# Performance work log

Hardware: AMD Instinct MI355X
Metric: run time of the kernel (lower is better)

The kernel has to match this reference:

```python
import jax, jax.numpy as jnp
import numpy as np

N_NODES = 100000
N_EDGES = 1600000
D_IN = 128
D_HID = 128
D_OUT = 40
N_LAYERS = 3
EPS = 1e-12


def setup_inputs() -> dict:
    key = jax.random.key(0)
    ks = jax.random.split(key, 12)
    s = 1.0 / np.sqrt(D_HID)
    return {
        "x": jax.random.normal(ks[0], (N_NODES, D_IN), jnp.float32),
        "edge_index": jax.random.randint(ks[1], (2, N_EDGES), 0, N_NODES, jnp.int64),
        "Wl": jax.random.uniform(ks[2], (N_LAYERS, D_HID, D_HID), jnp.float32, -s, s),
        "bl": jax.random.uniform(ks[3], (N_LAYERS, D_HID), jnp.float32, -s, s),
        "Wr": jax.random.uniform(ks[4], (N_LAYERS, D_HID, D_HID), jnp.float32, -s, s),
        "br": jax.random.uniform(ks[5], (N_LAYERS, D_HID), jnp.float32, -s, s),
        "W_post1": jax.random.uniform(ks[6], (D_HID, D_HID), jnp.float32, -s, s),
        "b_post1": jax.random.uniform(ks[7], (D_HID,), jnp.float32, -s, s),
        "W_post2": jax.random.uniform(ks[8], (D_OUT, D_HID), jnp.float32, -s, s),
        "b_post2": jax.random.uniform(ks[9], (D_OUT,), jnp.float32, -s, s),
    }


def reference(x, edge_index, Wl, bl, Wr, br, W_post1, b_post1, W_post2, b_post2):
    src, dst = edge_index[0], edge_index[1]
    n = x.shape[0]
    h = x
    for i in range(N_LAYERS):
        # scatter-add aggregation of neighbor features (MessagePassing aggr='add')
        prop = jax.ops.segment_sum(h[src], dst, num_segments=n)  # [N, D]
        out = h @ Wl[i].T + bl[i] + prop @ Wr[i].T + br[i]
        # F.normalize(out, p=2) along dim=1
        norm = jnp.linalg.norm(out, axis=1, keepdims=True)
        out = out / jnp.maximum(norm, EPS)
        h = jax.nn.relu(out)  # dropout p=0 -> identity
    h = h @ W_post1.T + b_post1
    h = h @ W_post2.T + b_post2
    return jax.nn.log_softmax(h, axis=1)
```

## Files before the change

### kernel.cpp

```cpp
#include <hip/hip_runtime.h>
#include <hip/hip_bf16.h>
#include <cstdint>
#include <cstddef>

#define NN 100000
#define DD 128
#define NE 1600000
#define NPB 196
#define NBUCK 511
#define BCAP 6144
#define BUCKCAP 4608
#define SCHUNK 8192

#if defined(__HIP_DEVICE_COMPILE__) && defined(__has_builtin)
# if __has_builtin(__builtin_amdgcn_cvt_pk_f32_fp8) && __has_builtin(__builtin_amdgcn_cvt_pk_fp8_f32)
#  define DEV_CVT8 1
# endif
#endif
#ifndef DEV_CVT8
# define DEV_CVT8 0
#endif

typedef short bf16x8 __attribute__((ext_vector_type(8)));
typedef float f32x4 __attribute__((ext_vector_type(4)));
typedef unsigned short u16;
typedef unsigned int u32;
typedef unsigned char u8;

__device__ inline float b2f(u16 u) {
    union { u32 i; float f; } c; c.i = ((u32)u) << 16; return c.f;
}
__device__ inline u16 f2b(float f) {
    __hip_bfloat16 h = __float2bfloat16(f);
    return *reinterpret_cast<u16*>(&h);
}

__device__ inline u32 enc1_fp8(float v) {
#if DEV_CVT8
    return 0;
#else
    float a = fabsf(v);
    if (a > 448.0f) a = 448.0f;
    u32 sgn = (v < 0.0f) ? 0x80u : 0u;
    if (a < 0.015625f) {
        int q = (int)rintf(a * 512.0f);
        return sgn | (u32)q;
    }
    int ex;
    float mant = frexpf(a, &ex);
    int m = (int)rintf(mant * 16.0f) - 8;
    int e = ex - 1 + 7;
    if (m == 8) { m = 0; e += 1; }
    if (e > 15) { e = 15; m = 6; }
    return sgn | ((u32)e << 3) | (u32)m;
#endif
}

__device__ inline u32 pack4_fp8(float a, float b, float c, float d) {
#if DEV_CVT8
    u32 r = 0;
    r = (u32)__builtin_amdgcn_cvt_pk_fp8_f32(a, b, (int)r, false);
    r = (u32)__builtin_amdgcn_cvt_pk_fp8_f32(c, d, (int)r, true);
    return r;
#else
    return enc1_fp8(a) | (enc1_fp8(b) << 8) | (enc1_fp8(c) << 16) | (enc1_fp8(d) << 24);
#endif
}

__device__ inline float dec1_fp8(u32 byte) {
    u32 lo = byte & 0x7Fu;
    union { u32 i; float f; } c;
    c.i = lo ? (((byte & 0x80u) << 24) | ((lo + 912u) << 20)) : 0u;
    return c.f;
}

__global__ __launch_bounds__(256)
void initcur_kernel(int* __restrict__ cur) {
    int t = blockIdx.x * 256 + threadIdx.x;
    if (t < NBUCK) cur[t] = t * BUCKCAP;
}

__global__ __launch_bounds__(256)
void bscatter_kernel(const int* __restrict__ ei, int* __restrict__ cursor,
                     u32* __restrict__ packed, int n_edges) {
    __shared__ int hist[NBUCK];
    const int tid = threadIdx.x;
    const int nchunks = (n_edges + SCHUNK - 1) / SCHUNK;
    for (int ch = blockIdx.x; ch < nchunks; ch += gridDim.x) {
        const int e0 = ch * SCHUNK;
        const int e1 = min(e0 + SCHUNK, n_edges);
        for (int i = tid; i < NBUCK; i += 256) hist[i] = 0;
        __syncthreads();
        for (int e = e0 + tid; e < e1; e += 256)
            atomicAdd(&hist[ei[n_edges + e] / NPB], 1);
        __syncthreads();
        for (int i = tid; i < NBUCK; i += 256) {
            int c = hist[i];
            hist[i] = (c > 0) ? atomicAdd(&cursor[i], c) : 0;
        }
        __syncthreads();
        for (int e = e0 + tid; e < e1; e += 256) {
            int s = ei[e];
            int d = ei[n_edges + e];
            int b = d / NPB;
            int ld = d - b * NPB;
            int pos = atomicAdd(&hist[b], 1);
            packed[pos] = ((u32)ld << 17) | (u32)s;
        }
        __syncthreads();
    }
}

__global__ __launch_bounds__(256)
void blocal_kernel(const u32* __restrict__ packed, const int* __restrict__ cursor,
                   int* __restrict__ row_ptr, int* __restrict__ rpe,
                   int* __restrict__ ssrc) {
    __shared__ int out_s[BCAP];
    __shared__ int cur_s[NPB];
    __shared__ int excl_s[NPB];
    __shared__ int ws[4];
    __shared__ int wexc[4];

    const int b = blockIdx.x;
    const int tid = threadIdx.x;
    const int lane = tid & 63, wv = tid >> 6;
    const int pbase = b * BUCKCAP;
    const int cnt = cursor[b] - pbase;

    if (tid < NPB) cur_s[tid] = 0;
    __syncthreads();
    for (int i = tid; i < cnt; i += 256)
        atomicAdd(&cur_s[packed[pbase + i] >> 17], 1);
    __syncthreads();

    int v = (tid < NPB) ? cur_s[tid] : 0;
    int inc = v;
    #pragma unroll
    for (int o = 1; o < 64; o <<= 1) {
        int u = __shfl_up(inc, o);
        if (lane >= o) inc += u;
    }
    if (lane == 63) ws[wv] = inc;
    __syncthreads();
    if (tid == 0) {
        int s = 0;
        #pragma unroll
        for (int k = 0; k < 4; ++k) { wexc[k] = s; s += ws[k]; }
    }
    __syncthreads();
    int excl = inc - v + wexc[wv];
    if (tid < NPB) excl_s[tid] = excl;
    int gnode = b * NPB + tid;
    if (tid < NPB && gnode < NN) {
        row_ptr[gnode] = pbase + excl;
        rpe[gnode] = pbase + excl + v;
    }
    __syncthreads();
    if (tid < NPB) cur_s[tid] = excl_s[tid];
    __syncthreads();

    if (cnt <= BCAP) {
        for (int i = tid; i < cnt; i += 256) {
            u32 p = packed[pbase + i];
            int pos = atomicAdd(&cur_s[p >> 17], 1);
            out_s[pos] = (int)(p & 0x1FFFF);
        }
        __syncthreads();
        for (int i = tid; i < cnt; i += 256) ssrc[pbase + i] = out_s[i];
    } else {
        for (int i = tid; i < cnt; i += 256) {
            u32 p = packed[pbase + i];
            int pos = atomicAdd(&cur_s[p >> 17], 1);
            ssrc[pbase + pos] = (int)(p & 0x1FFFF);
        }
    }
}

__global__ __launch_bounds__(256)
void cvt_x_kernel(const float* __restrict__ x, u16* __restrict__ xb,
                  u8* __restrict__ x8, long long n8) {
    long long t = (long long)blockIdx.x * blockDim.x + threadIdx.x;
    long long stride = (long long)gridDim.x * blockDim.x;
    for (; t < n8; t += stride) {
        float4 v0 = reinterpret_cast<const float4*>(x)[2 * t];
        float4 v1 = reinterpret_cast<const float4*>(x)[2 * t + 1];
        uint4 ob;
        ob.x = (u32)f2b(v0.x) | ((u32)f2b(v0.y) << 16);
        ob.y = (u32)f2b(v0.z) | ((u32)f2b(v0.w) << 16);
        ob.z = (u32)f2b(v1.x) | ((u32)f2b(v1.y) << 16);
        ob.w = (u32)f2b(v1.z) | ((u32)f2b(v1.w) << 16);
        reinterpret_cast<uint4*>(xb)[t] = ob;
        uint2 o8;
        o8.x = pack4_fp8(v0.x * 64.0f, v0.y * 64.0f, v0.z * 64.0f, v0.w * 64.0f);
        o8.y = pack4_fp8(v1.x * 64.0f, v1.y * 64.0f, v1.z * 64.0f, v1.w * 64.0f);
        reinterpret_cast<uint2*>(x8)[t] = o8;
    }
}

__global__ __launch_bounds__(256)
void cvt8_kernel(const u16* __restrict__ hb, u8* __restrict__ h8, int n8) {
    int t0 = blockIdx.x * 256 + threadIdx.x;
    int stride = gridDim.x * 256;
    for (int t = t0; t < n8; t += stride) {
        uint4 v = reinterpret_cast<const uint4*>(hb)[t];
        union { u32 i; float f; } c;
        float f0, f1, f2, f3, f4, f5, f6, f7;
        c.i = v.x << 16; f0 = c.f;  c.i = v.x & 0xffff0000u; f1 = c.f;
        c.i = v.y << 16; f2 = c.f;  c.i = v.y & 0xffff0000u; f3 = c.f;
        c.i = v.z << 16; f4 = c.f;  c.i = v.z & 0xffff0000u; f5 = c.f;
        c.i = v.w << 16; f6 = c.f;  c.i = v.w & 0xffff0000u; f7 = c.f;
        uint2 o;
        o.x = pack4_fp8(f0 * 64.0f, f1 * 64.0f, f2 * 64.0f, f3 * 64.0f);
        o.y = pack4_fp8(f4 * 64.0f, f5 * 64.0f, f6 * 64.0f, f7 * 64.0f);
        reinterpret_cast<uint2*>(h8)[t] = o;
    }
}

__global__ __launch_bounds__(256)
void cvt_w_kernel(const float* __restrict__ Wl, const float* __restrict__ Wr,
                  u16* __restrict__ Wcat) {
    int t = blockIdx.x * blockDim.x + threadIdx.x;
    const int NCAT = 3 * 128 * 256;
    if (t < NCAT) {
        int layer = t >> 15;
        int rem = t & 32767;
        int d = rem >> 8;
        int k = rem & 255;
        float v = (k < 128) ? Wl[layer * 16384 + d * 128 + k]
                            : Wr[layer * 16384 + d * 128 + (k - 128)];
        Wcat[t] = f2b(v);
    }
}

__global__ __launch_bounds__(256)
void wfuse_kernel(const float* __restrict__ W1f, const float* __restrict__ b1,
                  const float* __restrict__ W2, const float* __restrict__ b2,
                  u16* __restrict__ Wfb, float* __restrict__ bfuse) {
    int t = blockIdx.x * 256 + threadIdx.x;
    if (t < 48 * 128) {
        int l = t >> 7, k = t & 127;
        float s = 0.0f;
        if (l < 40) {
            for (int j = 0; j < 128; ++j)
                s += W2[l * 128 + j] * W1f[j * 128 + k];
        }
        Wfb[t] = f2b(s);
    }
    if (blockIdx.x == 0 && threadIdx.x < 40) {
        int l = threadIdx.x;
        float s = b2[l];
        for (int j = 0; j < 128; ++j) s += W2[l * 128 + j] * b1[j];
        bfuse[l] = s;
    }
}

#if DEV_CVT8
#define DEC8(q) do { \
    auto _p0 = __builtin_amdgcn_cvt_pk_f32_fp8((int)(q).x, false); \
    auto _p1 = __builtin_amdgcn_cvt_pk_f32_fp8((int)(q).x, true); \
    auto _p2 = __builtin_amdgcn_cvt_pk_f32_fp8((int)(q).y, false); \
    auto _p3 = __builtin_amdgcn_cvt_pk_f32_fp8((int)(q).y, true); \
    acc0 += _p0[0]; acc1 += _p0[1]; acc2 += _p1[0]; acc3 += _p1[1]; \
    acc4 += _p2[0]; acc5 += _p2[1]; acc6 += _p3[0]; acc7 += _p3[1]; \
} while (0)
#else
#define DEC8(q) do { \
    acc0 += dec1_fp8((q).x & 0xFFu); \
    acc1 += dec1_fp8(((q).x >> 8) & 0xFFu); \
    acc2 += dec1_fp8(((q).x >> 16) & 0xFFu); \
    acc3 += dec1_fp8((q).x >> 24); \
    acc4 += dec1_fp8((q).y & 0xFFu); \
    acc5 += dec1_fp8(((q).y >> 8) & 0xFFu); \
    acc6 += dec1_fp8(((q).y >> 16) & 0xFFu); \
    acc7 += dec1_fp8((q).y >> 24); \
} while (0)
#endif

__global__ __launch_bounds__(256)
void gather8_kernel(const u8* __restrict__ h8, const int* __restrict__ rp,
                    const int* __restrict__ rpe, const int* __restrict__ ssrc,
                    u16* __restrict__ prop, int n_nodes) {
    int wid = (blockIdx.x * blockDim.x + threadIdx.x) >> 6;
    int lane = threadIdx.x & 63;
    if (wid >= n_nodes) return;
    int beg = rp[wid], end = rpe[wid];
    int deg = end - beg;
    int nb = min(deg, 64);
    const int g = lane >> 4;
    const u8* hb = h8 + (lane & 15) * 8;

    float acc0 = 0, acc1 = 0, acc2 = 0, acc3 = 0;
    float acc4 = 0, acc5 = 0, acc6 = 0, acc7 = 0;

    int sv = (lane < nb) ? ssrc[beg + lane] : 0;

    int j = 0;
    for (; j + 15 < nb; j += 16) {
        int s0 = __shfl(sv, j + g);
        int s1 = __shfl(sv, j + 4 + g);
        int s2 = __shfl(sv, j + 8 + g);
        int s3 = __shfl(sv, j + 12 + g);
        uint2 v0 = *reinterpret_cast<const uint2*>(hb + (size_t)s0 * 128);
        uint2 v1 = *reinterpret_cast<const uint2*>(hb + (size_t)s1 * 128);
        uint2 v2 = *reinterpret_cast<const uint2*>(hb + (size_t)s2 * 128);
        uint2 v3 = *reinterpret_cast<const uint2*>(hb + (size_t)s3 * 128);
        DEC8(v0);
        DEC8(v1);
        DEC8(v2);
        DEC8(v3);
    }
    for (; j + 3 < nb; j += 4) {
        int s0 = __shfl(sv, j + g);
        uint2 v0 = *reinterpret_cast<const uint2*>(hb + (size_t)s0 * 128);
        DEC8(v0);
    }
    if (j < nb && g < nb - j) {
        int s0 = __shfl(sv, j + g);
        uint2 v0 = *reinterpret_cast<const uint2*>(hb + (size_t)s0 * 128);
        DEC8(v0);
    }
    for (int e = beg + 64 + g; e < end; e += 4) {
        int s0 = ssrc[e];
        uint2 v0 = *reinterpret_cast<const uint2*>(hb + (size_t)s0 * 128);
        DEC8(v0);
    }

    acc0 += __shfl_xor(acc0, 16); acc0 += __shfl_xor(acc0, 32);
    acc1 += __shfl_xor(acc1, 16); acc1 += __shfl_xor(acc1, 32);
    acc2 += __shfl_xor(acc2, 16); acc2 += __shfl_xor(acc2, 32);
    acc3 += __shfl_xor(acc3, 16); acc3 += __shfl_xor(acc3, 32);
    acc4 += __shfl_xor(acc4, 16); acc4 += __shfl_xor(acc4, 32);
    acc5 += __shfl_xor(acc5, 16); acc5 += __shfl_xor(acc5, 32);
    acc6 += __shfl_xor(acc6, 16); acc6 += __shfl_xor(acc6, 32);
    acc7 += __shfl_xor(acc7, 16); acc7 += __shfl_xor(acc7, 32);

    if (lane < 16) {
        const float us = 0.015625f;
        uint4 o;
        o.x = (u32)f2b(acc0 * us) | ((u32)f2b(acc1 * us) << 16);
        o.y = (u32)f2b(acc2 * us) | ((u32)f2b(acc3 * us) << 16);
        o.z = (u32)f2b(acc4 * us) | ((u32)f2b(acc5 * us) << 16);
        o.w = (u32)f2b(acc6 * us) | ((u32)f2b(acc7 * us) << 16);
        *reinterpret_cast<uint4*>(prop + (size_t)wid * DD + lane * 8) = o;
    }
}

__global__ __launch_bounds__(256)
void mfma_layer64(const u16* __restrict__ hin, const u16* __restrict__ prop,
                  const u16* __restrict__ Wc, const float* __restrict__ b1,
                  const float* __restrict__ b2, u16* __restrict__ out,
                  int n_nodes) {
    __shared__ char a_s[64 * 512];
    __shared__ float red_s[64][4];

    const int tid = threadIdx.x;
    const int w = tid >> 6;
    const int l = tid & 63;
    const int q = l >> 4;
    const int c16 = l & 15;

    bf16x8 bfrag[2][8];
    int col[2];
    float bias[2];
    #pragma unroll
    for (int t = 0; t < 2; ++t) {
        col[t] = w * 32 + t * 16 + c16;
        bias[t] = b1[col[t]] + b2[col[t]];
        #pragma unroll
        for (int kk = 0; kk < 8; ++kk)
            bfrag[t][kk] = *reinterpret_cast<const bf16x8*>(
                Wc + (size_t)col[t] * 256 + kk * 32 + q * 8);
    }

    const int base = blockIdx.x * 64;

    for (int ci = tid; ci < 2048; ci += 256) {
        int r = ci >> 5, c = ci & 31;
        int node = base + r;
        uint4 v = {0, 0, 0, 0};
        if (node < n_nodes) {
            const u16* src = (c < 16) ? (hin + (size_t)node * DD + c * 8)
                                      : (prop + (size_t)node * DD + (c - 16) * 8);
            v = *reinterpret_cast<const uint4*>(src);
        }
        *reinterpret_cast<uint4*>(a_s + r * 512 + ((c ^ (r & 7)) * 16)) = v;
    }
    __syncthreads();

    f32x4 acc[4][2] = {};
    #pragma unroll
    for (int kk = 0; kk < 8; ++kk) {
        int cc = kk * 4 + q;
        #pragma unroll
        for (int m = 0; m < 4; ++m) {
            int row = m * 16 + c16;
            bf16x8 a = *reinterpret_cast<const bf16x8*>(
                a_s + row * 512 + ((cc ^ (row & 7)) * 16));
            acc[m][0] = __builtin_amdgcn_mfma_f32_16x16x32_bf16(a, bfrag[0][kk], acc[m][0], 0, 0, 0);
            acc[m][1] = __builtin_amdgcn_mfma_f32_16x16x32_bf16(a, bfrag[1][kk], acc[m][1], 0, 0, 0);
        }
    }

    float vals[4][2][4];
    float ss[4][4];
    #pragma unroll
    for (int m = 0; m < 4; ++m) {
        #pragma unroll
        for (int reg = 0; reg < 4; ++reg) {
            float s = 0.0f;
            #pragma unroll
            for (int t = 0; t < 2; ++t) {
                float v = acc[m][t][reg] + bias[t];
                vals[m][t][reg] = v;
                s += v * v;
            }
            s += __shfl_xor(s, 1);
            s += __shfl_xor(s, 2);
            s += __shfl_xor(s, 4);
            s += __shfl_xor(s, 8);
            ss[m][reg] = s;
        }
    }
    if (c16 == 0) {
        #pragma unroll
        for (int m = 0; m < 4; ++m)
            #pragma unroll
            for (int reg = 0; reg < 4; ++reg)
                red_s[m * 16 + q * 4 + reg][w] = ss[m][reg];
    }
    __syncthreads();
    #pragma unroll
    for (int m = 0; m < 4; ++m) {
        #pragma unroll
        for (int reg = 0; reg < 4; ++reg) {
            int row = m * 16 + q * 4 + reg;
            float4 rr = *reinterpret_cast<float4*>(&red_s[row][0]);
            float tot = rr.x + rr.y + rr.z + rr.w;
            float rn = 1.0f / fmaxf(sqrtf(tot), 1e-12f);
            if (base + row < n_nodes) {
                #pragma unroll
                for (int t = 0; t < 2; ++t) {
                    float v = fmaxf(vals[m][t][reg] * rn, 0.0f);
                    out[(size_t)(base + row) * DD + col[t]] = f2b(v);
                }
            }
        }
    }
}

__global__ __launch_bounds__(256)
void postfused_kernel(const u16* __restrict__ hin, const u16* __restrict__ Wfb,
                      const float* __restrict__ bfuse, float* __restrict__ out,
                      int n_nodes) {
    __shared__ char a_s[64 * 256];
    const int tid = threadIdx.x;
    const int w = tid >> 6;
    const int l = tid & 63;
    const int q = l >> 4;
    const int c16 = l & 15;

    bf16x8 bfrag[3][4];
    float bias[3];
    int col[3];
    #pragma unroll
    for (int t = 0; t < 3; ++t) {
        col[t] = t * 16 + c16;
        bias[t] = (col[t] < 40) ? bfuse[col[t]] : 0.0f;
        #pragma unroll
        for (int kk = 0; kk < 4; ++kk)
            bfrag[t][kk] = *reinterpret_cast<const bf16x8*>(
                Wfb + col[t] * 128 + kk * 32 + q * 8);
    }

    const int base = blockIdx.x * 64;

    for (int ci = tid; ci < 1024; ci += 256) {
        int r = ci >> 4, c = ci & 15;
        uint4 v = {0, 0, 0, 0};
        if (base + r < n_nodes)
            v = *reinterpret_cast<const uint4*>(hin + (size_t)(base + r) * DD + c * 8);
        *reinterpret_cast<uint4*>(a_s + r * 256 + ((c ^ (r & 7)) * 16)) = v;
    }
    __syncthreads();

    f32x4 acc[3] = {};
    const int arow = w * 16 + c16;
    #pragma unroll
    for (int kk = 0; kk < 4; ++kk) {
        int cc = kk * 4 + q;
        bf16x8 a = *reinterpret_cast<const bf16x8*>(
            a_s + arow * 256 + ((cc ^ (arow & 7)) * 16));
        acc[0] = __builtin_amdgcn_mfma_f32_16x16x32_bf16(a, bfrag[0][kk], acc[0], 0, 0, 0);
        acc[1] = __builtin_amdgcn_mfma_f32_16x16x32_bf16(a, bfrag[1][kk], acc[1], 0, 0, 0);
        acc[2] = __builtin_amdgcn_mfma_f32_16x16x32_bf16(a, bfrag[2][kk], acc[2], 0, 0, 0);
    }

    #pragma unroll
    for (int reg = 0; reg < 4; ++reg) {
        int row = base + w * 16 + q * 4 + reg;
        float v[3];
        float m = -INFINITY;
        #pragma unroll
        for (int t = 0; t < 3; ++t) {
            v[t] = acc[t][reg] + bias[t];
            if (col[t] < 40) m = fmaxf(m, v[t]);
        }
        m = fmaxf(m, __shfl_xor(m, 1));
        m = fmaxf(m, __shfl_xor(m, 2));
        m = fmaxf(m, __shfl_xor(m, 4));
        m = fmaxf(m, __shfl_xor(m, 8));
        float s = 0.0f;
        #pragma unroll
        for (int t = 0; t < 3; ++t)
            if (col[t] < 40) s += expf(v[t] - m);
        s += __shfl_xor(s, 1);
        s += __shfl_xor(s, 2);
        s += __shfl_xor(s, 4);
        s += __shfl_xor(s, 8);
        float lg = logf(s);
        if (row < n_nodes) {
            #pragma unroll
            for (int t = 0; t < 3; ++t)
                if (col[t] < 40)
                    out[(size_t)row * 40 + col[t]] = v[t] - m - lg;
        }
    }
}

extern "C" void kernel_launch(void* const* d_in, const int* in_sizes, int n_in,
                              void* d_out, int out_size, void* d_ws, size_t ws_size,
                              hipStream_t stream) {
    const float* x   = (const float*)d_in[0];
    const int*   ei  = (const int*)d_in[1];
    const float* Wl  = (const float*)d_in[2];
    const float* bl  = (const float*)d_in[3];
    const float* Wr  = (const float*)d_in[4];
    const float* br  = (const float*)d_in[5];
    const float* W1f = (const float*)d_in[6];
    const float* b1  = (const float*)d_in[7];
    const float* W2  = (const float*)d_in[8];
    const float* b2  = (const float*)d_in[9];
    float* outp = (float*)d_out;

    u16* xb   = (u16*)d_ws;
    u16* P    = xb + (size_t)NN * DD;
    u16* bufA = P + (size_t)NN * DD;
    u16* bufB = bufA + (size_t)NN * DD;
    u8*  h8   = (u8*)(bufB + (size_t)NN * DD);
    u16* Wcat = (u16*)(h8 + (size_t)NN * 128);
    u16* Wfb  = Wcat + 3 * 128 * 256;
    float* bfuse = (float*)(Wfb + 8192);
    int* cursor  = (int*)(Wfb + 128 * 128);
    int* row_ptr = cursor + NBUCK + 1;
    int* rpe     = row_ptr + NN;
    int* ssrc    = rpe + NN;
    u32* packed  = (u32*)(ssrc + NBUCK * BUCKCAP);

    initcur_kernel<<<2, 256, 0, stream>>>(cursor);
    bscatter_kernel<<<(NE + SCHUNK - 1) / SCHUNK, 256, 0, stream>>>(
        ei, cursor, packed, NE);
    blocal_kernel<<<NBUCK, 256, 0, stream>>>(packed, cursor, row_ptr, rpe, ssrc);

    cvt_x_kernel<<<6250, 256, 0, stream>>>(x, xb, h8, (long long)NN * DD / 8);
    cvt_w_kernel<<<(3 * 128 * 256 + 255) / 256, 256, 0, stream>>>(Wl, Wr, Wcat);
    wfuse_kernel<<<24, 256, 0, stream>>>(W1f, b1, W2, b2, Wfb, bfuse);

    const int n_strips64 = (NN + 63) / 64;
    const int gather_grid = (NN * 64 + 255) / 256;
    const int n8 = NN * DD / 8;

    const u16* hcur = xb;
    u16* hnext;
    for (int i = 0; i < 3; ++i) {
        hnext = (i == 0) ? bufA : ((hcur == bufA) ? bufB : bufA);
        gather8_kernel<<<gather_grid, 256, 0, stream>>>(
            h8, row_ptr, rpe, ssrc, P, NN);
        mfma_layer64<<<n_strips64, 256, 0, stream>>>(
            hcur, P, Wcat + (size_t)i * 128 * 256,
            bl + (size_t)i * DD, br + (size_t)i * DD, hnext, NN);
        if (i < 2)
            cvt8_kernel<<<2048, 256, 0, stream>>>(hnext, h8, n8);
        hcur = hnext;
    }
    postfused_kernel<<<n_strips64, 256, 0, stream>>>(hcur, Wfb, bfuse, outp, NN);
}
```

Measured before the change: 312.7 us.

## Fuse fp8 emission into layer GEMM and load operands directly from global

The separate cvt8 pass is removed. Each layer GEMM now encodes its normalized ReLU output to scaled fp8 in shared memory and writes it out as the next layer's gather source. The GEMM also drops the LDS staging of the A tile and the preloaded weight fragments, and instead loads A rows and weight fragments straight from global memory inside the k loop. This saves a kernel launch and a full read and write of the bf16 activations, but the unstaged loads may be less coalesced and more latency bound.

```diff
diff --git a/kernel.cpp b/kernel.cpp
--- a/kernel.cpp
+++ b/kernel.cpp
@@ -35,10 +35,7 @@
     return *reinterpret_cast<u16*>(&h);
 }
 
-__device__ inline u32 enc1_fp8(float v) {
-#if DEV_CVT8
-    return 0;
-#else
+__device__ inline u32 enc1_fp8_sw(float v) {
     float a = fabsf(v);
     if (a > 448.0f) a = 448.0f;
     u32 sgn = (v < 0.0f) ? 0x80u : 0u;
@@ -53,7 +50,6 @@
     if (m == 8) { m = 0; e += 1; }
     if (e > 15) { e = 15; m = 6; }
     return sgn | ((u32)e << 3) | (u32)m;
-#endif
 }
 
 __device__ inline u32 pack4_fp8(float a, float b, float c, float d) {
@@ -63,7 +59,16 @@
     r = (u32)__builtin_amdgcn_cvt_pk_fp8_f32(c, d, (int)r, true);
     return r;
 #else
-    return enc1_fp8(a) | (enc1_fp8(b) << 8) | (enc1_fp8(c) << 16) | (enc1_fp8(d) << 24);
+    return enc1_fp8_sw(a) | (enc1_fp8_sw(b) << 8) | (enc1_fp8_sw(c) << 16)
+         | (enc1_fp8_sw(d) << 24);
+#endif
+}
+
+__device__ inline u8 enc1b_fp8(float v) {
+#if DEV_CVT8
+    return (u8)((u32)__builtin_amdgcn_cvt_pk_fp8_f32(v, v, 0, false) & 0xFFu);
+#else
+    return (u8)enc1_fp8_sw(v);
 #endif
 }
 
@@ -194,25 +199,6 @@
         o8.x = pack4_fp8(v0.x * 64.0f, v0.y * 64.0f, v0.z * 64.0f, v0.w * 64.0f);
         o8.y = pack4_fp8(v1.x * 64.0f, v1.y * 64.0f, v1.z * 64.0f, v1.w * 64.0f);
         reinterpret_cast<uint2*>(x8)[t] = o8;
-    }
-}
-
-__global__ __launch_bounds__(256)
-void cvt8_kernel(const u16* __restrict__ hb, u8* __restrict__ h8, int n8) {
-    int t0 = blockIdx.x * 256 + threadIdx.x;
-    int stride = gridDim.x * 256;
-    for (int t = t0; t < n8; t += stride) {
-        uint4 v = reinterpret_cast<const uint4*>(hb)[t];
-        union { u32 i; float f; } c;
-        float f0, f1, f2, f3, f4, f5, f6, f7;
-        c.i = v.x << 16; f0 = c.f;  c.i = v.x & 0xffff0000u; f1 = c.f;
-        c.i = v.y << 16; f2 = c.f;  c.i = v.y & 0xffff0000u; f3 = c.f;
-        c.i = v.z << 16; f4 = c.f;  c.i = v.z & 0xffff0000u; f5 = c.f;
-        c.i = v.w << 16; f6 = c.f;  c.i = v.w & 0xffff0000u; f7 = c.f;
-        uint2 o;
-        o.x = pack4_fp8(f0 * 64.0f, f1 * 64.0f, f2 * 64.0f, f3 * 64.0f);
-        o.y = pack4_fp8(f4 * 64.0f, f5 * 64.0f, f6 * 64.0f, f7 * 64.0f);
-        reinterpret_cast<uint2*>(h8)[t] = o;
     }
 }
 
@@ -345,13 +331,14 @@
     }
 }
 
-__global__ __launch_bounds__(256)
-void mfma_layer64(const u16* __restrict__ hin, const u16* __restrict__ prop,
-                  const u16* __restrict__ Wc, const float* __restrict__ b1,
-                  const float* __restrict__ b2, u16* __restrict__ out,
-                  int n_nodes) {
-    __shared__ char a_s[64 * 512];
+template<int EMIT8>
+__global__ __launch_bounds__(256)
+void mfma_layer_direct(const u16* __restrict__ hin, const u16* __restrict__ prop,
+                       const u16* __restrict__ Wc, const float* __restrict__ b1,
+                       const float* __restrict__ b2, u16* __restrict__ out,
+                       u8* __restrict__ h8out, int n_nodes) {
     __shared__ float red_s[64][4];
+    __shared__ u8 h8_s[EMIT8 ? 64 * 128 : 16];
 
     const int tid = threadIdx.x;
     const int w = tid >> 6;
@@ -359,45 +346,40 @@
     const int q = l >> 4;
     const int c16 = l & 15;
 
-    bf16x8 bfrag[2][8];
     int col[2];
     float bias[2];
     #pragma unroll
     for (int t = 0; t < 2; ++t) {
         col[t] = w * 32 + t * 16 + c16;
         bias[t] = b1[col[t]] + b2[col[t]];
-        #pragma unroll
-        for (int kk = 0; kk < 8; ++kk)
-            bfrag[t][kk] = *reinterpret_cast<const bf16x8*>(
-                Wc + (size_t)col[t] * 256 + kk * 32 + q * 8);
     }
 
     const int base = blockIdx.x * 64;
-
-    for (int ci = tid; ci < 2048; ci += 256) {
-        int r = ci >> 5, c = ci & 31;
-        int node = base + r;
-        uint4 v = {0, 0, 0, 0};
-        if (node < n_nodes) {
-            const u16* src = (c < 16) ? (hin + (size_t)node * DD + c * 8)
-                                      : (prop + (size_t)node * DD + (c - 16) * 8);
-            v = *reinterpret_cast<const uint4*>(src);
-        }
-        *reinterpret_cast<uint4*>(a_s + r * 512 + ((c ^ (r & 7)) * 16)) = v;
-    }
-    __syncthreads();
+    int node_m[4];
+    #pragma unroll
+    for (int m = 0; m < 4; ++m)
+        node_m[m] = min(base + m * 16 + c16, n_nodes - 1);
 
     f32x4 acc[4][2] = {};
     #pragma unroll
     for (int kk = 0; kk < 8; ++kk) {
-        int cc = kk * 4 + q;
+        const int cc = kk * 4 + q;
+        bf16x8 a[4];
         #pragma unroll
         for (int m = 0; m < 4; ++m) {
-            int row = m * 16 + c16;
-            bf16x8 a = *reinterpret_cast<const bf16x8*>(
-                a_s + row * 512 + ((cc ^ (row & 7)) * 16));
-            acc[m][0] = __builtin_amdgcn_mfma_f32_16x16x32_bf16(a, bfrag[0][kk], acc[m][0], 0, 0, 0);
-            acc[m][1] = __builtin_amdgcn_mfma_f32_16x16x32_bf16(a, bfrag[1][kk], acc[m][1], 0, 0, 0);
+            const u16* p = (kk < 4)
+                ? (hin + (size_t)node_m[m] * DD + cc * 8)
+                : (prop + (size_t)node_m[m] * DD + (cc - 16) * 8);
+            a[m] = *reinterpret_cast<const bf16x8*>(p);
+        }
+        bf16x8 bf0 = *reinterpret_cast<const bf16x8*>(
+            Wc + (size_t)col[0] * 256 + kk * 32 + q * 8);
+        bf16x8 bf1 = *reinterpret_cast<const bf16x8*>(
+            Wc + (size_t)col[1] * 256 + kk * 32 + q * 8);
+        #pragma unroll
+        for (int m = 0; m < 4; ++m) {
+            acc[m][0] = __builtin_amdgcn_mfma_f32_16x16x32_bf16(a[m], bf0, acc[m][0], 0, 0, 0);
+            acc[m][1] = __builtin_amdgcn_mfma_f32_16x16x32_bf16(a[m], bf1, acc[m][1], 0, 0, 0);
         }
     }
 
@@ -437,13 +419,25 @@
             float4 rr = *reinterpret_cast<float4*>(&red_s[row][0]);
             float tot = rr.x + rr.y + rr.z + rr.w;
             float rn = 1.0f / fmaxf(sqrtf(tot), 1e-12f);
-            if (base + row < n_nodes) {
-                #pragma unroll
-                for (int t = 0; t < 2; ++t) {
-                    float v = fmaxf(vals[m][t][reg] * rn, 0.0f);
+            bool alive = (base + row < n_nodes);
+            #pragma unroll
+            for (int t = 0; t < 2; ++t) {
+                float v = fmaxf(vals[m][t][reg] * rn, 0.0f);
+                if (alive)
                     out[(size_t)(base + row) * DD + col[t]] = f2b(v);
-                }
+                if (EMIT8)
+                    h8_s[row * 128 + col[t]] = enc1b_fp8(v * 64.0f);
             }
+        }
+    }
+    if (EMIT8) {
+        __syncthreads();
+        for (int i = tid; i < 512; i += 256) {
+            int row = i >> 3;
+            int node = base + row;
+            if (node < n_nodes)
+                reinterpret_cast<uint4*>(h8out + (size_t)node * 128)[i & 7] =
+                    reinterpret_cast<const uint4*>(h8_s)[i];
         }
     }
 }
@@ -567,7 +561,6 @@
 
     const int n_strips64 = (NN + 63) / 64;
     const int gather_grid = (NN * 64 + 255) / 256;
-    const int n8 = NN * DD / 8;
 
     const u16* hcur = xb;
     u16* hnext;
@@ -575,11 +568,15 @@
         hnext = (i == 0) ? bufA : ((hcur == bufA) ? bufB : bufA);
         gather8_kernel<<<gather_grid, 256, 0, stream>>>(
             h8, row_ptr, rpe, ssrc, P, NN);
-        mfma_layer64<<<n_strips64, 256, 0, stream>>>(
-            hcur, P, Wcat + (size_t)i * 128 * 256,
-            bl + (size_t)i * DD, br + (size_t)i * DD, hnext, NN);
-        if (i < 2)
-            cvt8_kernel<<<2048, 256, 0, stream>>>(hnext, h8, n8);
+        if (i < 2) {
+            mfma_layer_direct<1><<<n_strips64, 256, 0, stream>>>(
+                hcur, P, Wcat + (size_t)i * 128 * 256,
+                bl + (size_t)i * DD, br + (size_t)i * DD, hnext, h8, NN);
+        } else {
+            mfma_layer_direct<0><<<n_strips64, 256, 0, stream>>>(
+                hcur, P, Wcat + (size_t)i * 128 * 256,
+                bl + (size_t)i * DD, br + (size_t)i * DD, hnext, h8, NN);
+        }
         hcur = hnext;
     }
     postfused_kernel<<<n_strips64, 256, 0, stream>>>(hcur, Wfb, bfuse, outp, NN);
```

Result: slower. 350.5 us (+12.1%).

## Fuse neighbor gather into MFMA layer kernel, aggregating directly into LDS

Applied to the files above, without the earlier changes.

Merges the separate per-node fp8 gather kernel into the layer GEMM kernel: each block gathers and sums neighbor rows for its 64 nodes, with 16 lanes per node, and writes the bf16 aggregate straight into the swizzled shared-memory A tile. This removes the global round trip of the prop buffer and one kernel launch per layer. In exchange, each wave handles 4 nodes per pass, 16 at a time, with only 16 lanes each, so gather parallelism and latency hiding within a block fall and degree imbalance stalls the MFMA phase. Also renames the software fp8 encoder.

```diff
diff --git a/kernel.cpp b/kernel.cpp
--- a/kernel.cpp
+++ b/kernel.cpp
@@ -35,10 +35,7 @@
     return *reinterpret_cast<u16*>(&h);
 }
 
-__device__ inline u32 enc1_fp8(float v) {
-#if DEV_CVT8
-    return 0;
-#else
+__device__ inline u32 enc1_fp8_sw(float v) {
     float a = fabsf(v);
     if (a > 448.0f) a = 448.0f;
     u32 sgn = (v < 0.0f) ? 0x80u : 0u;
@@ -53,7 +50,6 @@
     if (m == 8) { m = 0; e += 1; }
     if (e > 15) { e = 15; m = 6; }
     return sgn | ((u32)e << 3) | (u32)m;
-#endif
 }
 
 __device__ inline u32 pack4_fp8(float a, float b, float c, float d) {
@@ -63,7 +59,8 @@
     r = (u32)__builtin_amdgcn_cvt_pk_fp8_f32(c, d, (int)r, true);
     return r;
 #else
-    return enc1_fp8(a) | (enc1_fp8(b) << 8) | (enc1_fp8(c) << 16) | (enc1_fp8(d) << 24);
+    return enc1_fp8_sw(a) | (enc1_fp8_sw(b) << 8) | (enc1_fp8_sw(c) << 16)
+         | (enc1_fp8_sw(d) << 24);
 #endif
 }
 
@@ -277,80 +274,12 @@
 #endif
 
 __global__ __launch_bounds__(256)
-void gather8_kernel(const u8* __restrict__ h8, const int* __restrict__ rp,
-                    const int* __restrict__ rpe, const int* __restrict__ ssrc,
-                    u16* __restrict__ prop, int n_nodes) {
-    int wid = (blockIdx.x * blockDim.x + threadIdx.x) >> 6;
-    int lane = threadIdx.x & 63;
-    if (wid >= n_nodes) return;
-    int beg = rp[wid], end = rpe[wid];
-    int deg = end - beg;
-    int nb = min(deg, 64);
-    const int g = lane >> 4;
-    const u8* hb = h8 + (lane & 15) * 8;
-
-    float acc0 = 0, acc1 = 0, acc2 = 0, acc3 = 0;
-    float acc4 = 0, acc5 = 0, acc6 = 0, acc7 = 0;
-
-    int sv = (lane < nb) ? ssrc[beg + lane] : 0;
-
-    int j = 0;
-    for (; j + 15 < nb; j += 16) {
-        int s0 = __shfl(sv, j + g);
-        int s1 = __shfl(sv, j + 4 + g);
-        int s2 = __shfl(sv, j + 8 + g);
-        int s3 = __shfl(sv, j + 12 + g);
-        uint2 v0 = *reinterpret_cast<const uint2*>(hb + (size_t)s0 * 128);
-        uint2 v1 = *reinterpret_cast<const uint2*>(hb + (size_t)s1 * 128);
-        uint2 v2 = *reinterpret_cast<const uint2*>(hb + (size_t)s2 * 128);
-        uint2 v3 = *reinterpret_cast<const uint2*>(hb + (size_t)s3 * 128);
-        DEC8(v0);
-        DEC8(v1);
-        DEC8(v2);
-        DEC8(v3);
-    }
-    for (; j + 3 < nb; j += 4) {
-        int s0 = __shfl(sv, j + g);
-        uint2 v0 = *reinterpret_cast<const uint2*>(hb + (size_t)s0 * 128);
-        DEC8(v0);
-    }
-    if (j < nb && g < nb - j) {
-        int s0 = __shfl(sv, j + g);
-        uint2 v0 = *reinterpret_cast<const uint2*>(hb + (size_t)s0 * 128);
-        DEC8(v0);
-    }
-    for (int e = beg + 64 + g; e < end; e += 4) {
-        int s0 = ssrc[e];
-        uint2 v0 = *reinterpret_cast<const uint2*>(hb + (size_t)s0 * 128);
-        DEC8(v0);
-    }
-
-    acc0 += __shfl_xor(acc0, 16); acc0 += __shfl_xor(acc0, 32);
-    acc1 += __shfl_xor(acc1, 16); acc1 += __shfl_xor(acc1, 32);
-    acc2 += __shfl_xor(acc2, 16); acc2 += __shfl_xor(acc2, 32);
-    acc3 += __shfl_xor(acc3, 16); acc3 += __shfl_xor(acc3, 32);
-    acc4 += __shfl_xor(acc4, 16); acc4 += __shfl_xor(acc4, 32);
-    acc5 += __shfl_xor(acc5, 16); acc5 += __shfl_xor(acc5, 32);
-    acc6 += __shfl_xor(acc6, 16); acc6 += __shfl_xor(acc6, 32);
-    acc7 += __shfl_xor(acc7, 16); acc7 += __shfl_xor(acc7, 32);
-
-    if (lane < 16) {
-        const float us = 0.015625f;
-        uint4 o;
-        o.x = (u32)f2b(acc0 * us) | ((u32)f2b(acc1 * us) << 16);
-        o.y = (u32)f2b(acc2 * us) | ((u32)f2b(acc3 * us) << 16);
-        o.z = (u32)f2b(acc4 * us) | ((u32)f2b(acc5 * us) << 16);
-        o.w = (u32)f2b(acc6 * us) | ((u32)f2b(acc7 * us) << 16);
-        *reinterpret_cast<uint4*>(prop + (size_t)wid * DD + lane * 8) = o;
-    }
-}
-
-__global__ __launch_bounds__(256)
-void mfma_layer64(const u16* __restrict__ hin, const u16* __restrict__ prop,
-                  const u16* __restrict__ Wc, const float* __restrict__ b1,
-                  const float* __restrict__ b2, u16* __restrict__ out,
-                  int n_nodes) {
-    __shared__ char a_s[64 * 512];
+void fused_layer(const u16* __restrict__ hin, const u8* __restrict__ h8,
+                 const int* __restrict__ rp, const int* __restrict__ rpe,
+                 const int* __restrict__ ssrc, const u16* __restrict__ Wc,
+                 const float* __restrict__ b1, const float* __restrict__ b2,
+                 u16* __restrict__ out, int n_nodes) {
+    __shared__ __attribute__((aligned(16))) char a_s[64 * 512];
     __shared__ float red_s[64][4];
 
     const int tid = threadIdx.x;
@@ -359,6 +288,63 @@
     const int q = l >> 4;
     const int c16 = l & 15;
 
+    const int base = blockIdx.x * 64;
+
+    for (int ci = tid; ci < 1024; ci += 256) {
+        int r = ci >> 4, c = ci & 15;
+        int node = base + r;
+        uint4 v = {0, 0, 0, 0};
+        if (node < n_nodes)
+            v = *reinterpret_cast<const uint4*>(hin + (size_t)node * DD + c * 8);
+        *reinterpret_cast<uint4*>(a_s + r * 512 + ((c ^ (r & 7)) * 16)) = v;
+    }
+
+    {
+        const int gb = l & 48;
+        const int cl = c16;
+        const float us = 0.015625f;
+        for (int pass = 0; pass < 4; ++pass) {
+            int r = w * 16 + pass * 4 + q;
+            int n = min(base + r, n_nodes - 1);
+            int beg = rp[n];
+            int deg = rpe[n] - beg;
+            float acc0 = 0, acc1 = 0, acc2 = 0, acc3 = 0;
+            float acc4 = 0, acc5 = 0, acc6 = 0, acc7 = 0;
+            for (int c0 = 0; c0 < deg; c0 += 16) {
+                int rem = deg - c0;
+                int sv = (cl < rem) ? ssrc[beg + c0 + cl] : 0;
+                #pragma unroll
+                for (int k = 0; k < 16; k += 4) {
+                    if (k >= rem) break;
+                    int s0 = __shfl(sv, gb | k);
+                    int s1 = __shfl(sv, gb | (k + 1));
+                    int s2 = __shfl(sv, gb | (k + 2));
+                    int s3 = __shfl(sv, gb | (k + 3));
+                    uint2 v0, v1 = {0, 0}, v2 = {0, 0}, v3 = {0, 0};
+                    v0 = *reinterpret_cast<const uint2*>(h8 + (size_t)s0 * 128 + cl * 8);
+                    if (k + 1 < rem)
+                        v1 = *reinterpret_cast<const uint2*>(h8 + (size_t)s1 * 128 + cl * 8);
+                    if (k + 2 < rem)
+                        v2 = *reinterpret_cast<const uint2*>(h8 + (size_t)s2 * 128 + cl * 8);
+                    if (k + 3 < rem)
+                        v3 = *reinterpret_cast<const uint2*>(h8 + (size_t)s3 * 128 + cl * 8);
+                    DEC8(v0);
+                    DEC8(v1);
+                    DEC8(v2);
+                    DEC8(v3);
+                }
+            }
+            uint4 o;
+            o.x = (u32)f2b(acc0 * us) | ((u32)f2b(acc1 * us) << 16);
+            o.y = (u32)f2b(acc2 * us) | ((u32)f2b(acc3 * us) << 16);
+            o.z = (u32)f2b(acc4 * us) | ((u32)f2b(acc5 * us) << 16);
+            o.w = (u32)f2b(acc6 * us) | ((u32)f2b(acc7 * us) << 16);
+            *reinterpret_cast<uint4*>(
+                a_s + r * 512 + (((16 + cl) ^ (r & 7)) * 16)) = o;
+        }
+    }
+    __syncthreads();
+
     bf16x8 bfrag[2][8];
     int col[2];
     float bias[2];
@@ -371,21 +357,6 @@
             bfrag[t][kk] = *reinterpret_cast<const bf16x8*>(
                 Wc + (size_t)col[t] * 256 + kk * 32 + q * 8);
     }
-
-    const int base = blockIdx.x * 64;
-
-    for (int ci = tid; ci < 2048; ci += 256) {
-        int r = ci >> 5, c = ci & 31;
-        int node = base + r;
-        uint4 v = {0, 0, 0, 0};
-        if (node < n_nodes) {
-            const u16* src = (c < 16) ? (hin + (size_t)node * DD + c * 8)
-                                      : (prop + (size_t)node * DD + (c - 16) * 8);
-            v = *reinterpret_cast<const uint4*>(src);
-        }
-        *reinterpret_cast<uint4*>(a_s + r * 512 + ((c ^ (r & 7)) * 16)) = v;
-    }
-    __syncthreads();
 
     f32x4 acc[4][2] = {};
     #pragma unroll
@@ -566,17 +537,14 @@
     wfuse_kernel<<<24, 256, 0, stream>>>(W1f, b1, W2, b2, Wfb, bfuse);
 
     const int n_strips64 = (NN + 63) / 64;
-    const int gather_grid = (NN * 64 + 255) / 256;
     const int n8 = NN * DD / 8;
 
     const u16* hcur = xb;
     u16* hnext;
     for (int i = 0; i < 3; ++i) {
         hnext = (i == 0) ? bufA : ((hcur == bufA) ? bufB : bufA);
-        gather8_kernel<<<gather_grid, 256, 0, stream>>>(
-            h8, row_ptr, rpe, ssrc, P, NN);
-        mfma_layer64<<<n_strips64, 256, 0, stream>>>(
-            hcur, P, Wcat + (size_t)i * 128 * 256,
+        fused_layer<<<n_strips64, 256, 0, stream>>>(
+            hcur, h8, row_ptr, rpe, ssrc, Wcat + (size_t)i * 128 * 256,
             bl + (size_t)i * DD, br + (size_t)i * DD, hnext, NN);
         if (i < 2)
             cvt8_kernel<<<2048, 256, 0, stream>>>(hnext, h8, n8);
```

New measurement: 290.7 us (median of 2 runs). -7.0%, faster.
